# Performance work log

Measured on AMD Instinct MI355X. Metric: run time of the kernel, lower is better.

The kernel has to match this reference:

```python
import jax, jax.numpy as jnp
import numpy as np

B = 8192
FEAT = 7680
HID = 512
LOC = 4
N_SCENES = 72


def setup_inputs() -> dict:
    key = jax.random.key(0)
    ks = jax.random.split(key, 12)
    s = lambda fan_in: 1.0 / np.sqrt(fan_in)
    inp = {
        "feat": jax.random.normal(ks[0], (B, FEAT), dtype=jnp.float32),
        "scene_idx": jax.random.randint(ks[1], (B,), 0, N_SCENES, dtype=jnp.int64),
        # visual_fc1: Linear(7680 -> 512)  (torch layout: W[out, in])
        "W1": jax.random.uniform(ks[2], (HID, FEAT), jnp.float32, -s(FEAT), s(FEAT)),
        "b1": jax.random.uniform(ks[3], (HID,), jnp.float32, -s(FEAT), s(FEAT)),
        # localization_fc: Linear(512 -> 512), ReLU, Linear(512 -> 4)
        "W2": jax.random.uniform(ks[4], (HID, HID), jnp.float32, -s(HID), s(HID)),
        "b2": jax.random.uniform(ks[5], (HID,), jnp.float32, -s(HID), s(HID)),
        "W3": jax.random.uniform(ks[6], (LOC, HID), jnp.float32, -s(HID), s(HID)),
        "b3": jax.random.uniform(ks[7], (LOC,), jnp.float32, -s(HID), s(HID)),
        # per-scene 2x2 affine (with bias) and 2x2 rotation (no bias)
        "xyW": jax.random.uniform(ks[8], (N_SCENES, 2, 2), jnp.float32, -s(2), s(2)),
        "xyb": jax.random.uniform(ks[9], (N_SCENES, 2), jnp.float32, -s(2), s(2)),
        "tW": jax.random.uniform(ks[10], (N_SCENES, 2, 2), jnp.float32, -s(2), s(2)),
    }
    return inp


def reference(feat, scene_idx, W1, b1, W2, b2, W3, b3, xyW, xyb, tW):
    # visual_fc1: Flatten (already flat) -> Linear -> ReLU
    h = jax.nn.relu(feat @ W1.T + b1)                 # [B, HID]
    # localization_fc: Linear -> ReLU -> Linear
    h = jax.nn.relu(h @ W2.T + b2)                    # [B, HID]
    shared = h @ W3.T + b3                            # [B, 4]
    # per-scene routed 2x2 linears: gather weights per sample, apply, "scatter" is
    # implicit since every row gets exactly one scene's transform.
    sidx = scene_idx.astype(jnp.int32)
    Wxy = xyW[sidx]                                   # [B, 2, 2]
    bxy = xyb[sidx]                                   # [B, 2]
    Wt = tW[sidx]                                     # [B, 2, 2]
    xy = jnp.einsum("boi,bi->bo", Wxy, shared[:, :2]) + bxy
    t = jnp.einsum("boi,bi->bo", Wt, shared[:, 2:])
    return jnp.concatenate([xy, t], axis=1)           # [B, 4]
```

## Files before the change

kernel.cpp:

```cpp
#include <hip/hip_runtime.h>
#include <stdint.h>
#include <stddef.h>

#define BROWS 8192
#define FEATK 7680
#define HIDN  512

typedef __attribute__((ext_vector_type(8))) __bf16 bf16x8;
typedef __attribute__((ext_vector_type(4))) float f32x4;

__device__ __forceinline__ unsigned short f2b(float f) {
  unsigned int u = __float_as_uint(f);
  unsigned int r = (u + 0x7FFFu + ((u >> 16) & 1u)) >> 16;
  return (unsigned short)r;
}

__global__ void cvt2_kernel(const float* __restrict__ s1, unsigned short* __restrict__ d1, int n1,
                            const float* __restrict__ s2, unsigned short* __restrict__ d2, int n2) {
  int i = blockIdx.x * blockDim.x + threadIdx.x;
  int stride = gridDim.x * blockDim.x;
  for (; i < n1 + n2; i += stride) {
    const float4* sp; ushort4* dp; int j;
    if (i < n1) { sp = (const float4*)s1; dp = (ushort4*)d1; j = i; }
    else        { sp = (const float4*)s2; dp = (ushort4*)d2; j = i - n1; }
    float4 v = sp[j];
    ushort4 o;
    o.x = f2b(v.x); o.y = f2b(v.y); o.z = f2b(v.z); o.w = f2b(v.w);
    dp[j] = o;
  }
}

#define K1_BM 128
#define K1_BK 32

__global__ __launch_bounds__(512, 1) void gemm1_fused_splitk(
    const float* __restrict__ A,
    const unsigned short* __restrict__ Bm,
    float* __restrict__ P,
    int M, int N, int K, int klen) {
  __shared__ unsigned short As[2][K1_BM * K1_BK];
  __shared__ unsigned short Bs[2][HIDN * K1_BK];

  const int tid  = threadIdx.x;
  const int lane = tid & 63;
  const int wid  = tid >> 6;
  const int wm   = wid >> 2;
  const int wn   = wid & 3;
  const int l16  = lane & 15;
  const int quad = lane >> 4;

  const int n       = blockIdx.x;
  const int kchunk  = n & 3;
  const int rowblk  = n >> 2;

  const int rowBase = rowblk * K1_BM;
  const int k_begin = kchunk * klen;
  const int nsteps  = klen / K1_BK;

  const int arow  = tid >> 3;
  const int akq   = tid & 7;
  const int brow0 = (wid * 64 + lane) >> 2;
  const int bkk   = (lane & 3) << 3;

  f32x4 acc[4][8] = {};

  {
    const int k0 = k_begin;
#pragma unroll
    for (int it = 0; it < 2; ++it) {
      int row = it * 64 + arow;
      float4 v = *(const float4*)(A + (size_t)(rowBase + row) * K + k0 + akq * 4);
      ushort4 o;
      o.x = f2b(v.x); o.y = f2b(v.y); o.z = f2b(v.z); o.w = f2b(v.w);
      *(ushort4*)(&As[0][row * K1_BK + akq * 4]) = o;
    }
#pragma unroll
    for (int it = 0; it < 4; ++it) {
      int cb  = it * 512 + wid * 64;
      int row = it * 128 + brow0;
      const unsigned short* gb = Bm + (size_t)row * K + (k0 + bkk);
      __builtin_amdgcn_global_load_lds(
          (const __attribute__((address_space(1))) void*)gb,
          (__attribute__((address_space(3))) void*)(&Bs[0][cb * 8]), 16, 0, 0);
    }
  }
  __syncthreads();

  int cur = 0;
  for (int t = 0; t < nsteps; ++t) {
    const int nxt = cur ^ 1;
    const bool hasNext = (t + 1 < nsteps);
    float4 va0, va1;

    if (hasNext) {
      const int kn = k_begin + (t + 1) * K1_BK;
      va0 = *(const float4*)(A + (size_t)(rowBase + arow) * K + kn + akq * 4);
      va1 = *(const float4*)(A + (size_t)(rowBase + 64 + arow) * K + kn + akq * 4);
#pragma unroll
      for (int it = 0; it < 4; ++it) {
        int cb  = it * 512 + wid * 64;
        int row = it * 128 + brow0;
        const unsigned short* gb = Bm + (size_t)row * K + (kn + bkk);
        __builtin_amdgcn_global_load_lds(
            (const __attribute__((address_space(1))) void*)gb,
            (__attribute__((address_space(3))) void*)(&Bs[nxt][cb * 8]), 16, 0, 0);
      }
      asm volatile("s_waitcnt vmcnt(6)" ::: "memory");
    } else {
      asm volatile("s_waitcnt vmcnt(0)" ::: "memory");
    }

    bf16x8 af[4], bfr[8];
#pragma unroll
    for (int mt = 0; mt < 4; ++mt)
      af[mt] = *(const bf16x8*)(&As[cur][(wm * 64 + mt * 16 + l16) * K1_BK + quad * 8]);
#pragma unroll
    for (int nt = 0; nt < 8; ++nt)
      bfr[nt] = *(const bf16x8*)(&Bs[cur][(wn * 128 + nt * 16 + l16) * K1_BK + quad * 8]);
#pragma unroll
    for (int mt = 0; mt < 4; ++mt)
#pragma unroll
      for (int nt = 0; nt < 8; ++nt)
        acc[mt][nt] = __builtin_amdgcn_mfma_f32_16x16x32_bf16(af[mt], bfr[nt], acc[mt][nt], 0, 0, 0);

    if (hasNext) {
      ushort4 o0, o1;
      o0.x = f2b(va0.x); o0.y = f2b(va0.y); o0.z = f2b(va0.z); o0.w = f2b(va0.w);
      o1.x = f2b(va1.x); o1.y = f2b(va1.y); o1.z = f2b(va1.z); o1.w = f2b(va1.w);
      *(ushort4*)(&As[nxt][arow * K1_BK + akq * 4]) = o0;
      *(ushort4*)(&As[nxt][(64 + arow) * K1_BK + akq * 4]) = o1;
    }
    asm volatile("s_waitcnt lgkmcnt(0)" ::: "memory");
    __builtin_amdgcn_s_barrier();
    cur = nxt;
  }

  float* outp = P + (size_t)kchunk * M * N;
#pragma unroll
  for (int mt = 0; mt < 4; ++mt) {
#pragma unroll
    for (int r = 0; r < 4; ++r) {
      int row = rowBase + wm * 64 + mt * 16 + quad * 4 + r;
      float* cp = outp + (size_t)row * N + wn * 128 + l16;
#pragma unroll
      for (int nt = 0; nt < 8; ++nt) cp[nt * 16] = acc[mt][nt][r];
    }
  }
}

__global__ __launch_bounds__(256) void reduce4_bias_relu(
    const float* __restrict__ P, const float* __restrict__ bias,
    unsigned short* __restrict__ H, int MN4, int N4) {
  int i = blockIdx.x * blockDim.x + threadIdx.x;
  if (i >= MN4) return;
  const float4* p = (const float4*)P;
  float4 a = p[i];
  float4 b = p[i + MN4];
  float4 c = p[i + 2 * MN4];
  float4 d = p[i + 3 * MN4];
  float4 bs = ((const float4*)bias)[i % N4];
  ushort4 o;
  o.x = f2b(fmaxf(a.x + b.x + c.x + d.x + bs.x, 0.0f));
  o.y = f2b(fmaxf(a.y + b.y + c.y + d.y + bs.y, 0.0f));
  o.z = f2b(fmaxf(a.z + b.z + c.z + d.z + bs.z, 0.0f));
  o.w = f2b(fmaxf(a.w + b.w + c.w + d.w + bs.w, 0.0f));
  ((ushort4*)H)[i] = o;
}

#define K2_BM 64
#define K2_BN 128
#define K2_BK 64

__global__ __launch_bounds__(256, 2) void gemm2_bias_relu(
    const unsigned short* __restrict__ A,
    const unsigned short* __restrict__ Bm,
    const float* __restrict__ bias,
    unsigned short* __restrict__ C,
    int M, int N, int K) {
  __shared__ unsigned short As[2][K2_BM * K2_BK];
  __shared__ unsigned short Bs[2][K2_BN * K2_BK];
  const int tid  = threadIdx.x;
  const int lane = tid & 63;
  const int wid  = tid >> 6;
  const int wm   = wid >> 1;
  const int wn   = wid & 1;
  const int l16  = lane & 15;
  const int quad = lane >> 4;
  const int rowBase = blockIdx.y * K2_BM;
  const int colBase = blockIdx.x * K2_BN;

  const int srow = tid >> 3;
  const int skk  = (tid & 7) << 3;

  f32x4 acc[2][4] = {};
  const int nsteps = K / K2_BK;

#pragma unroll
  for (int it = 0; it < 2; ++it) {
    int cb  = it * 256 + wid * 64;
    int row = it * 32 + srow;
    const unsigned short* ga = A + (size_t)(rowBase + row) * K + skk;
    __builtin_amdgcn_global_load_lds(
        (const __attribute__((address_space(1))) void*)ga,
        (__attribute__((address_space(3))) void*)(&As[0][cb * 8]), 16, 0, 0);
  }
#pragma unroll
  for (int it = 0; it < 4; ++it) {
    int cb  = it * 256 + wid * 64;
    int row = it * 32 + srow;
    const unsigned short* gb = Bm + (size_t)(colBase + row) * K + skk;
    __builtin_amdgcn_global_load_lds(
        (const __attribute__((address_space(1))) void*)gb,
        (__attribute__((address_space(3))) void*)(&Bs[0][cb * 8]), 16, 0, 0);
  }
  __syncthreads();

  int cur = 0;
  for (int t = 0; t < nsteps; ++t) {
    const int nxt = cur ^ 1;
    if (t + 1 < nsteps) {
      const int kn = (t + 1) * K2_BK;
#pragma unroll
      for (int it = 0; it < 2; ++it) {
        int cb  = it * 256 + wid * 64;
        int row = it * 32 + srow;
        const unsigned short* ga = A + (size_t)(rowBase + row) * K + kn + skk;
        __builtin_amdgcn_global_load_lds(
            (const __attribute__((address_space(1))) void*)ga,
            (__attribute__((address_space(3))) void*)(&As[nxt][cb * 8]), 16, 0, 0);
      }
#pragma unroll
      for (int it = 0; it < 4; ++it) {
        int cb  = it * 256 + wid * 64;
        int row = it * 32 + srow;
        const unsigned short* gb = Bm + (size_t)(colBase + row) * K + kn + skk;
        __builtin_amdgcn_global_load_lds(
            (const __attribute__((address_space(1))) void*)gb,
            (__attribute__((address_space(3))) void*)(&Bs[nxt][cb * 8]), 16, 0, 0);
      }
      asm volatile("s_waitcnt vmcnt(6)" ::: "memory");
    } else {
      asm volatile("s_waitcnt vmcnt(0)" ::: "memory");
    }
#pragma unroll
    for (int kk = 0; kk < K2_BK; kk += 32) {
      bf16x8 af[2], bfr[4];
#pragma unroll
      for (int mt = 0; mt < 2; ++mt)
        af[mt] = *(const bf16x8*)(&As[cur][(wm * 32 + mt * 16 + l16) * K2_BK + kk + quad * 8]);
#pragma unroll
      for (int nt = 0; nt < 4; ++nt)
        bfr[nt] = *(const bf16x8*)(&Bs[cur][(wn * 64 + nt * 16 + l16) * K2_BK + kk + quad * 8]);
#pragma unroll
      for (int mt = 0; mt < 2; ++mt)
#pragma unroll
        for (int nt = 0; nt < 4; ++nt)
          acc[mt][nt] = __builtin_amdgcn_mfma_f32_16x16x32_bf16(af[mt], bfr[nt], acc[mt][nt], 0, 0, 0);
    }
    asm volatile("s_waitcnt lgkmcnt(0)" ::: "memory");
    __builtin_amdgcn_s_barrier();
    cur = nxt;
  }

  float bvals[4];
#pragma unroll
  for (int nt = 0; nt < 4; ++nt) bvals[nt] = bias[colBase + wn * 64 + nt * 16 + l16];
#pragma unroll
  for (int mt = 0; mt < 2; ++mt) {
#pragma unroll
    for (int r = 0; r < 4; ++r) {
      int row = rowBase + wm * 32 + mt * 16 + quad * 4 + r;
      unsigned short* cp = C + (size_t)row * N + colBase + wn * 64 + l16;
#pragma unroll
      for (int nt = 0; nt < 4; ++nt) {
        float v = fmaxf(acc[mt][nt][r] + bvals[nt], 0.0f);
        cp[nt * 16] = f2b(v);
      }
    }
  }
}

__global__ __launch_bounds__(256) void head_kernel(
    const unsigned short* __restrict__ h2,
    const float* __restrict__ W3,
    const float* __restrict__ b3,
    const int* __restrict__ sidx,
    const float* __restrict__ xyW,
    const float* __restrict__ xyb,
    const float* __restrict__ tW,
    float* __restrict__ out) {
  int wave = (blockIdx.x * blockDim.x + threadIdx.x) >> 6;
  int lane = threadIdx.x & 63;
  if (wave >= BROWS) return;

  bf16x8 hv = *(const bf16x8*)(h2 + (size_t)wave * 512 + lane * 8);
  float hf[8];
#pragma unroll
  for (int j = 0; j < 8; ++j) hf[j] = (float)hv[j];

  float s[4];
#pragma unroll
  for (int o = 0; o < 4; ++o) {
    const float* wrow = W3 + o * 512 + lane * 8;
    float4 w0 = ((const float4*)wrow)[0];
    float4 w1 = ((const float4*)wrow)[1];
    float a = hf[0] * w0.x + hf[1] * w0.y + hf[2] * w0.z + hf[3] * w0.w +
              hf[4] * w1.x + hf[5] * w1.y + hf[6] * w1.z + hf[7] * w1.w;
#pragma unroll
    for (int off = 32; off > 0; off >>= 1) a += __shfl_down(a, off, 64);
    s[o] = a;
  }

  if (lane == 0) {
#pragma unroll
    for (int o = 0; o < 4; ++o) s[o] += b3[o];
    int sc = sidx[wave];
    const float* wx = xyW + sc * 4;
    const float* bx = xyb + sc * 2;
    const float* wt = tW + sc * 4;
    float o0 = wx[0] * s[0] + wx[1] * s[1] + bx[0];
    float o1 = wx[2] * s[0] + wx[3] * s[1] + bx[1];
    float o2 = wt[0] * s[2] + wt[1] * s[3];
    float o3 = wt[2] * s[2] + wt[3] * s[3];
    ((float4*)out)[wave] = make_float4(o0, o1, o2, o3);
  }
}

#define WS_W1B   0UL
#define WS_W2B   7864320UL
#define WS_H1    8388608UL
#define WS_H2    16777216UL
#define WS_PART  25165824UL
#define WS_NEED  92274688UL

extern "C" void kernel_launch(void* const* d_in, const int* in_sizes, int n_in,
                              void* d_out, int out_size, void* d_ws, size_t ws_size,
                              hipStream_t stream) {
  const float* feat = (const float*)d_in[0];
  const int*   sidx = (const int*)d_in[1];
  const float* W1   = (const float*)d_in[2];
  const float* b1   = (const float*)d_in[3];
  const float* W2   = (const float*)d_in[4];
  const float* b2   = (const float*)d_in[5];
  const float* W3   = (const float*)d_in[6];
  const float* b3   = (const float*)d_in[7];
  const float* xyW  = (const float*)d_in[8];
  const float* xyb  = (const float*)d_in[9];
  const float* tW   = (const float*)d_in[10];
  float* out = (float*)d_out;

  if (ws_size < WS_NEED) return;

  char* ws = (char*)d_ws;
  unsigned short* W1B  = (unsigned short*)(ws + WS_W1B);
  unsigned short* W2B  = (unsigned short*)(ws + WS_W2B);
  unsigned short* h1   = (unsigned short*)(ws + WS_H1);
  unsigned short* h2   = (unsigned short*)(ws + WS_H2);
  float*          part = (float*)(ws + WS_PART);

  cvt2_kernel<<<576, 256, 0, stream>>>(W1, W1B, (HIDN * FEATK) / 4,
                                       W2, W2B, (HIDN * HIDN) / 4);

  gemm1_fused_splitk<<<256, 512, 0, stream>>>(
      feat, W1B, part, BROWS, HIDN, FEATK, FEATK / 4);
  reduce4_bias_relu<<<(BROWS * HIDN / 4 + 255) / 256, 256, 0, stream>>>(
      part, b1, h1, BROWS * HIDN / 4, HIDN / 4);

  gemm2_bias_relu<<<dim3(HIDN / K2_BN, BROWS / K2_BM), 256, 0, stream>>>(
      h1, W2B, b2, h2, BROWS, HIDN, HIDN);

  head_kernel<<<(BROWS * 64) / 256, 256, 0, stream>>>(
      h2, W3, b3, sidx, xyW, xyb, tW, out);
}
```

Baseline: 470.8 us.

## Triple-buffer B tiles and interleave loads with MFMA phases in gemm1

Moves the B-operand LDS buffer from double to triple buffering so B tiles are prefetched two K-steps ahead. The main loop is split into four phases, each issuing a slice of LDS reads and global-to-LDS DMA before a block of MFMAs run at raised wave priority. The aim is to hide global-memory latency and LDS read latency behind matrix work. In exchange it adds extra LDS usage and many more block barriers per step, and relies on hand-counted vmcnt waits being correct.

```diff
diff --git a/kernel.cpp b/kernel.cpp
--- a/kernel.cpp
+++ b/kernel.cpp
@@ -33,13 +33,23 @@
 #define K1_BM 128
 #define K1_BK 32
 
+#define K1_BDMA(buf, kcol, it)                                                   \
+  do {                                                                           \
+    int cb_  = (it) * 512 + wid * 64;                                            \
+    int row_ = (it) * 128 + brow0;                                               \
+    const unsigned short* gb_ = Bm + (size_t)row_ * K + ((kcol) + bkk);          \
+    __builtin_amdgcn_global_load_lds(                                            \
+        (const __attribute__((address_space(1))) void*)gb_,                      \
+        (__attribute__((address_space(3))) void*)(&Bs[buf][cb_ * 8]), 16, 0, 0); \
+  } while (0)
+
 __global__ __launch_bounds__(512, 1) void gemm1_fused_splitk(
     const float* __restrict__ A,
     const unsigned short* __restrict__ Bm,
     float* __restrict__ P,
     int M, int N, int K, int klen) {
   __shared__ unsigned short As[2][K1_BM * K1_BK];
-  __shared__ unsigned short Bs[2][HIDN * K1_BK];
+  __shared__ unsigned short Bs[3][HIDN * K1_BK];
 
   const int tid  = threadIdx.x;
   const int lane = tid & 63;
@@ -52,7 +62,6 @@
   const int n       = blockIdx.x;
   const int kchunk  = n & 3;
   const int rowblk  = n >> 2;
-
   const int rowBase = rowblk * K1_BM;
   const int k_begin = kchunk * klen;
   const int nsteps  = klen / K1_BK;
@@ -65,74 +74,105 @@
   f32x4 acc[4][8] = {};
 
   {
-    const int k0 = k_begin;
-#pragma unroll
-    for (int it = 0; it < 2; ++it) {
-      int row = it * 64 + arow;
-      float4 v = *(const float4*)(A + (size_t)(rowBase + row) * K + k0 + akq * 4);
-      ushort4 o;
-      o.x = f2b(v.x); o.y = f2b(v.y); o.z = f2b(v.z); o.w = f2b(v.w);
-      *(ushort4*)(&As[0][row * K1_BK + akq * 4]) = o;
-    }
-#pragma unroll
-    for (int it = 0; it < 4; ++it) {
-      int cb  = it * 512 + wid * 64;
-      int row = it * 128 + brow0;
-      const unsigned short* gb = Bm + (size_t)row * K + (k0 + bkk);
-      __builtin_amdgcn_global_load_lds(
-          (const __attribute__((address_space(1))) void*)gb,
-          (__attribute__((address_space(3))) void*)(&Bs[0][cb * 8]), 16, 0, 0);
-    }
-  }
-  __syncthreads();
-
-  int cur = 0;
+    float4 va0 = *(const float4*)(A + (size_t)(rowBase + arow) * K + k_begin + akq * 4);
+    float4 va1 = *(const float4*)(A + (size_t)(rowBase + 64 + arow) * K + k_begin + akq * 4);
+    K1_BDMA(0, k_begin, 0); K1_BDMA(0, k_begin, 1); K1_BDMA(0, k_begin, 2); K1_BDMA(0, k_begin, 3);
+    const int k1c = k_begin + K1_BK;
+    K1_BDMA(1, k1c, 0); K1_BDMA(1, k1c, 1); K1_BDMA(1, k1c, 2); K1_BDMA(1, k1c, 3);
+    asm volatile("s_waitcnt vmcnt(8)" ::: "memory");
+    ushort4 o0, o1;
+    o0.x = f2b(va0.x); o0.y = f2b(va0.y); o0.z = f2b(va0.z); o0.w = f2b(va0.w);
+    o1.x = f2b(va1.x); o1.y = f2b(va1.y); o1.z = f2b(va1.z); o1.w = f2b(va1.w);
+    *(ushort4*)(&As[0][arow * K1_BK + akq * 4]) = o0;
+    *(ushort4*)(&As[0][(64 + arow) * K1_BK + akq * 4]) = o1;
+    asm volatile("s_waitcnt vmcnt(4) lgkmcnt(0)" ::: "memory");
+    __builtin_amdgcn_s_barrier();
+  }
+
+  int cur3 = 0, b2 = 2, curA = 0;
   for (int t = 0; t < nsteps; ++t) {
-    const int nxt = cur ^ 1;
     const bool hasNext = (t + 1 < nsteps);
+    const bool hasB2   = (t + 2 < nsteps);
+    const int  nxtA    = curA ^ 1;
+    const int  kn      = k_begin + (t + 1) * K1_BK;
+    const int  kn2     = k_begin + (t + 2) * K1_BK;
     float4 va0, va1;
-
+    bf16x8 af[4], bfr[8];
+
+#pragma unroll
+    for (int mt = 0; mt < 4; ++mt)
+      af[mt] = *(const bf16x8*)(&As[curA][(wm * 64 + mt * 16 + l16) * K1_BK + quad * 8]);
+    bfr[0] = *(const bf16x8*)(&Bs[cur3][(wn * 128 + 0 * 16 + l16) * K1_BK + quad * 8]);
+    bfr[1] = *(const bf16x8*)(&Bs[cur3][(wn * 128 + 1 * 16 + l16) * K1_BK + quad * 8]);
     if (hasNext) {
-      const int kn = k_begin + (t + 1) * K1_BK;
       va0 = *(const float4*)(A + (size_t)(rowBase + arow) * K + kn + akq * 4);
       va1 = *(const float4*)(A + (size_t)(rowBase + 64 + arow) * K + kn + akq * 4);
-#pragma unroll
-      for (int it = 0; it < 4; ++it) {
-        int cb  = it * 512 + wid * 64;
-        int row = it * 128 + brow0;
-        const unsigned short* gb = Bm + (size_t)row * K + (kn + bkk);
-        __builtin_amdgcn_global_load_lds(
-            (const __attribute__((address_space(1))) void*)gb,
-            (__attribute__((address_space(3))) void*)(&Bs[nxt][cb * 8]), 16, 0, 0);
-      }
-      asm volatile("s_waitcnt vmcnt(6)" ::: "memory");
-    } else {
-      asm volatile("s_waitcnt vmcnt(0)" ::: "memory");
-    }
-
-    bf16x8 af[4], bfr[8];
-#pragma unroll
-    for (int mt = 0; mt < 4; ++mt)
-      af[mt] = *(const bf16x8*)(&As[cur][(wm * 64 + mt * 16 + l16) * K1_BK + quad * 8]);
-#pragma unroll
-    for (int nt = 0; nt < 8; ++nt)
-      bfr[nt] = *(const bf16x8*)(&Bs[cur][(wn * 128 + nt * 16 + l16) * K1_BK + quad * 8]);
-#pragma unroll
-    for (int mt = 0; mt < 4; ++mt)
-#pragma unroll
-      for (int nt = 0; nt < 8; ++nt)
-        acc[mt][nt] = __builtin_amdgcn_mfma_f32_16x16x32_bf16(af[mt], bfr[nt], acc[mt][nt], 0, 0, 0);
-
+    }
+    __builtin_amdgcn_s_barrier();
+    asm volatile("s_waitcnt lgkmcnt(0)" ::: "memory");
+    __builtin_amdgcn_s_setprio(1);
+#pragma unroll
+    for (int mt = 0; mt < 4; ++mt) {
+      acc[mt][0] = __builtin_amdgcn_mfma_f32_16x16x32_bf16(af[mt], bfr[0], acc[mt][0], 0, 0, 0);
+      acc[mt][1] = __builtin_amdgcn_mfma_f32_16x16x32_bf16(af[mt], bfr[1], acc[mt][1], 0, 0, 0);
+    }
+    __builtin_amdgcn_s_setprio(0);
+    __builtin_amdgcn_s_barrier();
+
+    bfr[2] = *(const bf16x8*)(&Bs[cur3][(wn * 128 + 2 * 16 + l16) * K1_BK + quad * 8]);
+    bfr[3] = *(const bf16x8*)(&Bs[cur3][(wn * 128 + 3 * 16 + l16) * K1_BK + quad * 8]);
+    if (hasB2) { K1_BDMA(b2, kn2, 0); K1_BDMA(b2, kn2, 1); }
+    __builtin_amdgcn_s_barrier();
+    asm volatile("s_waitcnt lgkmcnt(0)" ::: "memory");
+    __builtin_amdgcn_s_setprio(1);
+#pragma unroll
+    for (int mt = 0; mt < 4; ++mt) {
+      acc[mt][2] = __builtin_amdgcn_mfma_f32_16x16x32_bf16(af[mt], bfr[2], acc[mt][2], 0, 0, 0);
+      acc[mt][3] = __builtin_amdgcn_mfma_f32_16x16x32_bf16(af[mt], bfr[3], acc[mt][3], 0, 0, 0);
+    }
+    __builtin_amdgcn_s_setprio(0);
+    __builtin_amdgcn_s_barrier();
+
+    bfr[4] = *(const bf16x8*)(&Bs[cur3][(wn * 128 + 4 * 16 + l16) * K1_BK + quad * 8]);
+    bfr[5] = *(const bf16x8*)(&Bs[cur3][(wn * 128 + 5 * 16 + l16) * K1_BK + quad * 8]);
+    if (hasB2) { K1_BDMA(b2, kn2, 2); }
+    __builtin_amdgcn_s_barrier();
+    asm volatile("s_waitcnt lgkmcnt(0)" ::: "memory");
+    __builtin_amdgcn_s_setprio(1);
+#pragma unroll
+    for (int mt = 0; mt < 4; ++mt) {
+      acc[mt][4] = __builtin_amdgcn_mfma_f32_16x16x32_bf16(af[mt], bfr[4], acc[mt][4], 0, 0, 0);
+      acc[mt][5] = __builtin_amdgcn_mfma_f32_16x16x32_bf16(af[mt], bfr[5], acc[mt][5], 0, 0, 0);
+    }
+    __builtin_amdgcn_s_setprio(0);
+    __builtin_amdgcn_s_barrier();
+
+    bfr[6] = *(const bf16x8*)(&Bs[cur3][(wn * 128 + 6 * 16 + l16) * K1_BK + quad * 8]);
+    bfr[7] = *(const bf16x8*)(&Bs[cur3][(wn * 128 + 7 * 16 + l16) * K1_BK + quad * 8]);
+    if (hasB2) { K1_BDMA(b2, kn2, 3); }
     if (hasNext) {
+      if (hasB2) { asm volatile("s_waitcnt vmcnt(4)" ::: "memory"); }
+      else       { asm volatile("s_waitcnt vmcnt(0)" ::: "memory"); }
       ushort4 o0, o1;
       o0.x = f2b(va0.x); o0.y = f2b(va0.y); o0.z = f2b(va0.z); o0.w = f2b(va0.w);
       o1.x = f2b(va1.x); o1.y = f2b(va1.y); o1.z = f2b(va1.z); o1.w = f2b(va1.w);
-      *(ushort4*)(&As[nxt][arow * K1_BK + akq * 4]) = o0;
-      *(ushort4*)(&As[nxt][(64 + arow) * K1_BK + akq * 4]) = o1;
+      *(ushort4*)(&As[nxtA][arow * K1_BK + akq * 4]) = o0;
+      *(ushort4*)(&As[nxtA][(64 + arow) * K1_BK + akq * 4]) = o1;
     }
     asm volatile("s_waitcnt lgkmcnt(0)" ::: "memory");
     __builtin_amdgcn_s_barrier();
-    cur = nxt;
+    __builtin_amdgcn_s_setprio(1);
+#pragma unroll
+    for (int mt = 0; mt < 4; ++mt) {
+      acc[mt][6] = __builtin_amdgcn_mfma_f32_16x16x32_bf16(af[mt], bfr[6], acc[mt][6], 0, 0, 0);
+      acc[mt][7] = __builtin_amdgcn_mfma_f32_16x16x32_bf16(af[mt], bfr[7], acc[mt][7], 0, 0, 0);
+    }
+    __builtin_amdgcn_s_setprio(0);
+    __builtin_amdgcn_s_barrier();
+
+    curA = nxtA;
+    cur3 = (cur3 == 2) ? 0 : cur3 + 1;
+    b2   = (b2 == 2) ? 0 : b2 + 1;
   }
 
   float* outp = P + (size_t)kchunk * M * N;
```

New measurement: 456.6 us. 1.03x faster.
